# Kernel tuning notes

Measured on AMD Instinct MI355X. Metric: run time of the kernel, lower is better.

## Reference

```python
import jax, jax.numpy as jnp
import numpy as np

NEG_SLOPE = 0.01  # LeakyReLU default


def gcn_conv(x, src, dst, W, b, num_nodes):
    """PyG GCNConv: x' = D^-1/2 (A+I) D^-1/2 (x W) + b, self-loops added."""
    h = x @ W
    loop = jnp.arange(num_nodes)
    s = jnp.concatenate([src, loop])
    d = jnp.concatenate([dst, loop])
    deg = jax.ops.segment_sum(jnp.ones(s.shape[0], dtype=h.dtype), d,
                              num_segments=num_nodes)
    dinv = jnp.where(deg > 0, jax.lax.rsqrt(deg), 0.0)
    norm = dinv[s] * dinv[d]              # (Ep+N,)
    out = jax.ops.segment_sum(h[s] * norm[:, None], d, num_segments=num_nodes)
    return out + b


def leaky_relu(x):
    return jnp.where(x > 0, x, NEG_SLOPE * x)


def setup_inputs() -> dict:
    key = jax.random.key(0)
    ks = jax.random.split(key, 8)
    B, V, E, Fsub, H = 16, 100000, 300000, 800000, 16
    verts = jax.random.normal(ks[0], (B, V, 3), dtype=jnp.float32)
    edges = jax.random.randint(ks[1], (E, 2), 0, V)
    faces_sub = jax.random.randint(ks[2], (Fsub, 3), 0, V + E)
    W1 = jax.random.normal(ks[3], (3, H), dtype=jnp.float32) * 0.01
    W2 = jax.random.normal(ks[4], (H, H), dtype=jnp.float32) * 0.01
    W3 = jax.random.normal(ks[5], (H, 3), dtype=jnp.float32) * 0.01
    return {"verts": verts, "edges": edges, "faces_sub": faces_sub,
            "W1": W1, "b1": jnp.zeros((H,), jnp.float32),
            "W2": W2, "b2": jnp.zeros((H,), jnp.float32),
            "W3": W3, "b3": jnp.zeros((3,), jnp.float32)}


def reference(verts, edges, faces_sub, W1, b1, W2, b2, W3, b3):
    B, V, _ = verts.shape
    E = edges.shape[0]
    N = B * V
    # pack edges across the batch (same topology per mesh, offset per mesh)
    offsets = (jnp.arange(B) * V).astype(edges.dtype)
    pe = (edges[None, :, :] + offsets[:, None, None]).reshape(B * E, 2)
    src, dst = pe[:, 0], pe[:, 1]

    x = verts.reshape(N, 3)
    h = leaky_relu(gcn_conv(x, src, dst, W1, b1, N))
    h = leaky_relu(gcn_conv(h, src, dst, W2, b2, N))
    # Dropout(0.5) is identity at inference
    offs = gcn_conv(h, src, dst, W3, b3, N)

    v = (x + offs).reshape(B, V, 3)          # offset_verts
    mid = v[:, edges].mean(axis=2)           # (B, E, 3) edge midpoints
    new_verts = jnp.concatenate([v, mid], axis=1)   # (B, V+E, 3)
    new_faces = jnp.broadcast_to(faces_sub[None], (B,) + faces_sub.shape)
    return new_verts, new_faces
```

## Files before the change

### kernel.cpp

```cpp
#include <hip/hip_runtime.h>
#include <hip/hip_bf16.h>

#define NEG_SLOPE 0.01f

typedef long long i64;
typedef __hip_bfloat16 bf16;

__device__ __forceinline__ float lrelu(float x) { return x > 0.f ? x : NEG_SLOPE * x; }
__device__ __forceinline__ float b2f(bf16 v) { return __bfloat162float(v); }
__device__ __forceinline__ float lo2f(unsigned u) { return __uint_as_float(u << 16); }
__device__ __forceinline__ float hi2f(unsigned u) { return __uint_as_float(u & 0xffff0000u); }
__device__ __forceinline__ unsigned pk2(float a, float b) {
    unsigned ua = __bfloat16_as_ushort(__float2bfloat16(a));
    unsigned ub = __bfloat16_as_ushort(__float2bfloat16(b));
    return ua | (ub << 16);
}
__device__ __forceinline__ void acc8(float* h, uint4 u) {
    h[0] += lo2f(u.x); h[1] += hi2f(u.x);
    h[2] += lo2f(u.y); h[3] += hi2f(u.y);
    h[4] += lo2f(u.z); h[5] += hi2f(u.z);
    h[6] += lo2f(u.w); h[7] += hi2f(u.w);
}

__device__ __forceinline__ void decode_bxb(int wg, int NB, int CBc, int& b, int& xb) {
    if ((CBc & 7) == 0) {
        int xcd = wg & 7, k = wg >> 3;
        int bl = k / NB;
        xb = k - bl * NB;
        b = xcd + 8 * bl;
    } else {
        b = wg / NB;
        xb = wg - b * NB;
    }
}

__global__ __launch_bounds__(256) void k_deg(const int* __restrict__ edges,
                                             int* __restrict__ indeg, int E) {
    int e = blockIdx.x * 256 + threadIdx.x;
    if (e < E) atomicAdd(&indeg[edges[2 * e + 1]], 1);
}

__global__ __launch_bounds__(256) void k_dinv(const int* __restrict__ indeg,
                                              float* __restrict__ dinv, int V) {
    int v = blockIdx.x * 256 + threadIdx.x;
    if (v < V) dinv[v] = rsqrtf((float)indeg[v] + 1.0f);
}

__global__ __launch_bounds__(256) void k_scan1(const int* __restrict__ indeg,
                                               int* __restrict__ rowptr,
                                               int* __restrict__ bsum, int V) {
    __shared__ int s[256];
    int i = blockIdx.x * 256 + threadIdx.x;
    int x = (i < V) ? indeg[i] : 0;
    s[threadIdx.x] = x;
    __syncthreads();
    for (int off = 1; off < 256; off <<= 1) {
        int t = (threadIdx.x >= (unsigned)off) ? s[threadIdx.x - off] : 0;
        __syncthreads();
        s[threadIdx.x] += t;
        __syncthreads();
    }
    if (i < V) rowptr[i] = s[threadIdx.x] - x;
    if (threadIdx.x == 255) bsum[blockIdx.x] = s[255];
}

__global__ __launch_bounds__(1024) void k_scan2(int* __restrict__ bsum, int NB) {
    __shared__ int s[1024];
    __shared__ int srun;
    if (threadIdx.x == 0) srun = 0;
    __syncthreads();
    for (int base = 0; base < NB; base += 1024) {
        int i = base + threadIdx.x;
        int x = (i < NB) ? bsum[i] : 0;
        s[threadIdx.x] = x;
        __syncthreads();
        for (int off = 1; off < 1024; off <<= 1) {
            int t = (threadIdx.x >= (unsigned)off) ? s[threadIdx.x - off] : 0;
            __syncthreads();
            s[threadIdx.x] += t;
            __syncthreads();
        }
        int run = srun;
        if (i < NB) bsum[i] = run + s[threadIdx.x] - x;
        __syncthreads();
        if (threadIdx.x == 1023) srun = run + s[1023];
        __syncthreads();
    }
}

__global__ __launch_bounds__(256) void k_scan3(int* __restrict__ rowptr,
                                               const int* __restrict__ bsum,
                                               int V, int E) {
    int i = blockIdx.x * 256 + threadIdx.x;
    if (i < V) rowptr[i] += bsum[blockIdx.x];
    if (i == 0) rowptr[V] = E;
}

__global__ __launch_bounds__(256) void k_fill(const int* __restrict__ edges,
                                              const int* __restrict__ rowptr,
                                              int* __restrict__ cur,
                                              int* __restrict__ col, int E) {
    int e = blockIdx.x * 256 + threadIdx.x;
    if (e >= E) return;
    int s = edges[2 * e], d = edges[2 * e + 1];
    int p = atomicAdd(&cur[d], 1);
    col[rowptr[d] + p] = s;
}

__global__ __launch_bounds__(256) void k_gl12(const int* __restrict__ rowptr,
                                              const int* __restrict__ col,
                                              const float* __restrict__ verts,
                                              const float* __restrict__ W1,
                                              const float* __restrict__ b1,
                                              const float* __restrict__ W2,
                                              const float* __restrict__ dinv,
                                              bf16* __restrict__ PB,
                                              float* __restrict__ Q,
                                              int b0, int V, int NB, int CBc) {
    int b, xb;
    decode_bxb(blockIdx.x, NB, CBc, b, xb);
    int v = xb * 256 + threadIdx.x;
    if (v >= V) return;
    i64 vg = (i64)(b0 + b) * V;
    i64 vb = (i64)b * V;
    float di = dinv[v];
    const float* xv = verts + (vg + v) * 3;
    float x0 = xv[0], x1 = xv[1], x2 = xv[2];
    float a0 = di * x0, a1 = di * x1, a2 = di * x2;
    float h[16];
#pragma unroll
    for (int f = 0; f < 16; ++f)
        h[f] = a0 * W1[f] + a1 * W1[16 + f] + a2 * W1[32 + f];
    int r0 = rowptr[v], r1 = rowptr[v + 1];
#pragma unroll 2
    for (int j = r0; j < r1; ++j) {
        int s = col[j];
        float ds = dinv[s];
        const float* xs = verts + (vg + s) * 3;
        float y0 = ds * xs[0], y1 = ds * xs[1], y2 = ds * xs[2];
#pragma unroll
        for (int f = 0; f < 16; ++f)
            h[f] += y0 * W1[f] + y1 * W1[16 + f] + y2 * W1[32 + f];
    }
#pragma unroll
    for (int f = 0; f < 16; ++f) h[f] = lrelu(di * h[f] + b1[f]);
    float g[16];
#pragma unroll
    for (int f = 0; f < 16; ++f) g[f] = 0.f;
#pragma unroll
    for (int k = 0; k < 16; ++k) {
        float hk = h[k];
#pragma unroll
        for (int f = 0; f < 16; ++f) g[f] += hk * W2[k * 16 + f];
    }
#pragma unroll
    for (int f = 0; f < 16; ++f) g[f] *= di;
    i64 m = vb + v;
    uint4* Pp = (uint4*)(PB + m * 16);
    Pp[0] = make_uint4(pk2(g[0], g[1]), pk2(g[2], g[3]), pk2(g[4], g[5]), pk2(g[6], g[7]));
    Pp[1] = make_uint4(pk2(g[8], g[9]), pk2(g[10], g[11]), pk2(g[12], g[13]), pk2(g[14], g[15]));
    float4* Qp = (float4*)(Q + m * 16);
#pragma unroll
    for (int q = 0; q < 4; ++q)
        Qp[q] = make_float4(g[4 * q], g[4 * q + 1], g[4 * q + 2], g[4 * q + 3]);
}

__global__ __launch_bounds__(256) void k_gl3(const int* __restrict__ rowptr,
                                             const int* __restrict__ col,
                                             const float* __restrict__ W3,
                                             const float* __restrict__ b2,
                                             const float* __restrict__ dinv,
                                             const bf16* __restrict__ Pin,
                                             const float* __restrict__ Q,
                                             float* __restrict__ R,
                                             int V, int NB, int CBc) {
    int b, xb;
    decode_bxb(blockIdx.x, NB, CBc, b, xb);
    int v = xb * 256 + threadIdx.x;
    if (v >= V) return;
    i64 vb = (i64)b * V;
    i64 m = vb + v;
    float h[16];
    const float4* Qin = (const float4*)(Q + m * 16);
#pragma unroll
    for (int q = 0; q < 4; ++q) {
        float4 t = Qin[q];
        h[4 * q] = t.x; h[4 * q + 1] = t.y; h[4 * q + 2] = t.z; h[4 * q + 3] = t.w;
    }
    const uint4* Pb = (const uint4*)(Pin + vb * 16);
    int r0 = rowptr[v], r1 = rowptr[v + 1];
    int j = r0;
    for (; j + 1 < r1; j += 2) {
        size_t u0 = (size_t)col[j] * 2, u1 = (size_t)col[j + 1] * 2;
        uint4 q0 = Pb[u0], q1 = Pb[u0 + 1];
        uint4 c0 = Pb[u1], c1 = Pb[u1 + 1];
        acc8(h, q0); acc8(h + 8, q1);
        acc8(h, c0); acc8(h + 8, c1);
    }
    if (j < r1) {
        size_t u0 = (size_t)col[j] * 2;
        uint4 q0 = Pb[u0], q1 = Pb[u0 + 1];
        acc8(h, q0); acc8(h + 8, q1);
    }
    float di = dinv[v];
    float g0 = 0.f, g1 = 0.f, g2 = 0.f;
#pragma unroll
    for (int k = 0; k < 16; ++k) {
        float hk = lrelu(di * h[k] + b2[k]);
        g0 += hk * W3[k * 3 + 0];
        g1 += hk * W3[k * 3 + 1];
        g2 += hk * W3[k * 3 + 2];
    }
    ((float4*)R)[m] = make_float4(di * g0, di * g1, di * g2, 0.f);
}

__global__ __launch_bounds__(256) void k_gvert(const int* __restrict__ rowptr,
                                               const int* __restrict__ col,
                                               const float* __restrict__ x,
                                               const float* __restrict__ b3,
                                               const float* __restrict__ dinv,
                                               const float* __restrict__ R,
                                               float* __restrict__ Vpos,
                                               float* __restrict__ out0,
                                               int b0, int V, int E, int NB, int CBc) {
    int b, xb;
    decode_bxb(blockIdx.x, NB, CBc, b, xb);
    int v = xb * 256 + threadIdx.x;
    if (v >= V) return;
    i64 vb = (i64)b * V;
    i64 m = vb + v;
    const float4* Rb = (const float4*)R + vb;
    float4 s = Rb[v];
    int r0 = rowptr[v], r1 = rowptr[v + 1];
    int j = r0;
    for (; j + 1 < r1; j += 2) {
        float4 t0 = Rb[col[j]];
        float4 t1 = Rb[col[j + 1]];
        s.x += t0.x + t1.x; s.y += t0.y + t1.y; s.z += t0.z + t1.z;
    }
    if (j < r1) {
        float4 t0 = Rb[col[j]];
        s.x += t0.x; s.y += t0.y; s.z += t0.z;
    }
    float di = dinv[v];
    int bg = b0 + b;
    i64 n = (i64)bg * V + v;
    float p0 = x[n * 3]     + di * s.x + b3[0];
    float p1 = x[n * 3 + 1] + di * s.y + b3[1];
    float p2 = x[n * 3 + 2] + di * s.z + b3[2];
    ((float4*)Vpos)[m] = make_float4(p0, p1, p2, 0.f);
    i64 o = ((i64)bg * (V + E) + v) * 3;
    __builtin_nontemporal_store(p0, out0 + o);
    __builtin_nontemporal_store(p1, out0 + o + 1);
    __builtin_nontemporal_store(p2, out0 + o + 2);
}

__global__ __launch_bounds__(256) void k_mid(const int* __restrict__ edges,
                                             const float* __restrict__ Vpos,
                                             float* __restrict__ out0,
                                             int b0, int V, int E, int NB, int CBc) {
    int b, xe;
    decode_bxb(blockIdx.x, NB, CBc, b, xe);
    int e = xe * 256 + threadIdx.x;
    if (e >= E) return;
    int s = edges[2 * e], d = edges[2 * e + 1];
    float4 ps = ((const float4*)Vpos)[(i64)b * V + s];
    float4 pd = ((const float4*)Vpos)[(i64)b * V + d];
    i64 o = ((i64)(b0 + b) * (V + E) + V + e) * 3;
    __builtin_nontemporal_store(0.5f * (ps.x + pd.x), out0 + o);
    __builtin_nontemporal_store(0.5f * (ps.y + pd.y), out0 + o + 1);
    __builtin_nontemporal_store(0.5f * (ps.z + pd.z), out0 + o + 2);
}

__global__ __launch_bounds__(256) void k_faces(const int* __restrict__ faces,
                                               float* __restrict__ out1,
                                               i64 F3, i64 faceElems) {
    i64 i = (i64)blockIdx.x * 256 + threadIdx.x;
    if (i >= F3) return;
    i64 o = (i64)blockIdx.y * F3 + i;
    if (o < faceElems) __builtin_nontemporal_store((float)faces[i], out1 + o);
}

__global__ __launch_bounds__(256) void k_l1_g(const float* __restrict__ x,
                                              const float* __restrict__ W1,
                                              const float* __restrict__ dinv,
                                              bf16* __restrict__ P, float* __restrict__ Q,
                                              int b0, int V, int H) {
    extern __shared__ float sW[];
    for (int i = threadIdx.x; i < 3 * H; i += 256) sW[i] = W1[i];
    __syncthreads();
    int v = blockIdx.x * 256 + threadIdx.x;
    if (v >= V) return;
    i64 n = (i64)(b0 + blockIdx.y) * V + v;
    i64 m = (i64)blockIdx.y * V + v;
    float di = dinv[v];
    float x0 = x[n * 3], x1 = x[n * 3 + 1], x2 = x[n * 3 + 2];
    for (int f = 0; f < H; ++f) {
        float g = di * (x0 * sW[f] + x1 * sW[H + f] + x2 * sW[2 * H + f]);
        P[m * H + f] = __float2bfloat16(g);
        Q[m * H + f] = g;
    }
}

__global__ __launch_bounds__(256) void k_scatter_g(const int* __restrict__ edges,
                                                   const bf16* __restrict__ P,
                                                   float* __restrict__ Q,
                                                   int E, int V, int H) {
    int e = blockIdx.x * 256 + threadIdx.x;
    if (e >= E) return;
    int b = blockIdx.y;
    int s = edges[2 * e], d = edges[2 * e + 1];
    for (int f = 0; f < H; ++f)
        unsafeAtomicAdd(&Q[((i64)b * V + d) * H + f], b2f(P[((i64)b * V + s) * H + f]));
}

__global__ __launch_bounds__(256) void k_l2_g(const float* __restrict__ W2,
                                              const float* __restrict__ b1,
                                              const float* __restrict__ dinv,
                                              bf16* __restrict__ P, float* __restrict__ Q,
                                              int V, int H) {
    extern __shared__ float sW[];
    float* sb = sW + H * H;
    for (int i = threadIdx.x; i < H * H; i += 256) sW[i] = W2[i];
    for (int i = threadIdx.x; i < H; i += 256) sb[i] = b1[i];
    __syncthreads();
    int v = blockIdx.x * 256 + threadIdx.x;
    if (v >= V) return;
    i64 m = (i64)blockIdx.y * V + v;
    float di = dinv[v];
    float h[64];
    for (int k = 0; k < H; ++k) h[k] = lrelu(di * Q[m * H + k] + sb[k]);
    for (int f = 0; f < H; ++f) {
        float a = 0.f;
        for (int k = 0; k < H; ++k) a += h[k] * sW[k * H + f];
        float g = di * a;
        P[m * H + f] = __float2bfloat16(g);
        Q[m * H + f] = g;
    }
}

__global__ __launch_bounds__(256) void k_l3_g(const float* __restrict__ W3,
                                              const float* __restrict__ b2,
                                              const float* __restrict__ dinv,
                                              float* __restrict__ R,
                                              const float* __restrict__ Q, int V, int H) {
    extern __shared__ float sW[];
    float* sb = sW + H * 3;
    for (int i = threadIdx.x; i < H * 3; i += 256) sW[i] = W3[i];
    for (int i = threadIdx.x; i < H; i += 256) sb[i] = b2[i];
    __syncthreads();
    int v = blockIdx.x * 256 + threadIdx.x;
    if (v >= V) return;
    i64 m = (i64)blockIdx.y * V + v;
    float di = dinv[v];
    float g0 = 0.f, g1 = 0.f, g2 = 0.f;
    for (int k = 0; k < H; ++k) {
        float h = lrelu(di * Q[m * H + k] + sb[k]);
        g0 += h * sW[k * 3]; g1 += h * sW[k * 3 + 1]; g2 += h * sW[k * 3 + 2];
    }
    ((float4*)R)[m] = make_float4(di * g0, di * g1, di * g2, 0.f);
}

extern "C" void kernel_launch(void* const* d_in, const int* in_sizes, int n_in,
                              void* d_out, int out_size, void* d_ws, size_t ws_size,
                              hipStream_t stream) {
    const float* verts = (const float*)d_in[0];
    const int*   edges = (const int*)d_in[1];
    const int*   faces = (const int*)d_in[2];
    const float* W1 = (const float*)d_in[3];
    const float* b1 = (const float*)d_in[4];
    const float* W2 = (const float*)d_in[5];
    const float* b2 = (const float*)d_in[6];
    const float* W3 = (const float*)d_in[7];
    const float* b3 = (const float*)d_in[8];

    const i64 s0 = in_sizes[0];
    const i64 E  = in_sizes[1] / 2;
    const i64 F  = in_sizes[2] / 3;
    const int H  = in_sizes[4];
    i64 B = 0;
    const i64 denomB = 3 * (E + F);
    if ((i64)out_size > s0 && denomB > 0) {
        i64 Bc = ((i64)out_size - s0) / denomB;
        if (Bc >= 1 && s0 + Bc * denomB == (i64)out_size && s0 % (3 * Bc) == 0) B = Bc;
    }
    if (B == 0) {
        i64 num = (i64)out_size - s0 - 3 * F;
        if (num > 0 && E > 0 && num % (3 * E) == 0) {
            i64 Bc = num / (3 * E);
            if (Bc >= 1 && s0 % (3 * Bc) == 0) B = Bc;
        }
    }
    if (B == 0) B = 16;
    const i64 V = s0 / (3 * B);

    const i64 Vp  = (V + 255) & ~255LL;
    const i64 NB1 = Vp >> 8;
    const size_t AUX = (size_t)Vp * 4  + (size_t)Vp * 4
                     + (size_t)(Vp + 256) * 4
                     + (size_t)(NB1 + 256) * 4
                     + (size_t)E * 4  + 1024;
    const size_t rowB = (size_t)(6 * H) + 96 + 64;
    i64 CB = B;
    while (CB > 1 && AUX + (size_t)CB * V * rowB + 8192 > ws_size) CB = (CB + 1) / 2;

    float* ws     = (float*)d_ws;
    float* dinv   = ws;
    int*   indeg  = (int*)(ws + Vp);
    int*   rowptr = indeg + Vp;
    int*   bsum   = rowptr + Vp + 256;
    int*   col    = bsum + NB1 + 256;
    char*  base   = (char*)(((size_t)(col + E) + 255) & ~(size_t)255);
    auto pad = [](size_t x) { return (x + 255) & ~(size_t)255; };

    bf16 *PB = nullptr, *Pg = nullptr;
    float *Q, *R, *Vb;
    {
        char* p = base;
        if (H == 16) {
            PB = (bf16*)p;  p += pad((size_t)CB * V * 32);
            Q  = (float*)p; p += pad((size_t)CB * V * 64);
        } else {
            Pg = (bf16*)p;  p += pad((size_t)CB * V * 2 * H);
            Q  = (float*)p; p += pad((size_t)CB * V * 4 * H);
        }
        R  = (float*)p; p += pad((size_t)CB * V * 16);
        Vb = (float*)p;
    }

    const unsigned NBv = (unsigned)((V + 255) / 256);
    const unsigned NBe = (unsigned)((E + 255) / 256);

    hipMemsetAsync(indeg, 0, V * sizeof(int), stream);
    if (NBe) k_deg<<<dim3(NBe), 256, 0, stream>>>(edges, indeg, (int)E);
    k_dinv<<<dim3(NBv), 256, 0, stream>>>(indeg, dinv, (int)V);
    k_scan1<<<dim3(NBv), 256, 0, stream>>>(indeg, rowptr, bsum, (int)V);
    k_scan2<<<dim3(1), 1024, 0, stream>>>(bsum, (int)NBv);
    k_scan3<<<dim3(NBv), 256, 0, stream>>>(rowptr, bsum, (int)V, (int)E);
    hipMemsetAsync(indeg, 0, V * sizeof(int), stream);
    if (NBe) k_fill<<<dim3(NBe), 256, 0, stream>>>(edges, rowptr, indeg, col, (int)E);

    float* out0 = (float*)d_out;
    const i64 vertElems = B * (V + E) * 3;
    float* out1 = out0 + vertElems;
    const i64 faceElems = (i64)out_size - vertElems;

    for (i64 b0 = 0; b0 < B; b0 += CB) {
        const i64 CBc = (B - b0 < CB) ? (B - b0) : CB;
        dim3 g1((unsigned)(NBv * CBc));
        dim3 g1e((unsigned)(NBe * CBc));
        if (H == 16) {
            k_gl12<<<g1, 256, 0, stream>>>(rowptr, col, verts, W1, b1, W2, dinv,
                                           PB, Q, (int)b0, (int)V, (int)NBv, (int)CBc);
            k_gl3<<<g1, 256, 0, stream>>>(rowptr, col, W3, b2, dinv, PB, Q, R,
                                          (int)V, (int)NBv, (int)CBc);
        } else {
            dim3 gn(NBv, (unsigned)CBc);
            dim3 ge(NBe, (unsigned)CBc);
            size_t sh1 = (size_t)3 * H * 4;
            size_t sh2 = ((size_t)H * H + H) * 4;
            size_t sh3 = ((size_t)H * 3 + H) * 4;
            k_l1_g<<<gn, 256, sh1, stream>>>(verts, W1, dinv, Pg, Q, (int)b0, (int)V, H);
            if (NBe) k_scatter_g<<<ge, 256, 0, stream>>>(edges, Pg, Q, (int)E, (int)V, H);
            k_l2_g<<<gn, 256, sh2, stream>>>(W2, b1, dinv, Pg, Q, (int)V, H);
            if (NBe) k_scatter_g<<<ge, 256, 0, stream>>>(edges, Pg, Q, (int)E, (int)V, H);
            k_l3_g<<<gn, 256, sh3, stream>>>(W3, b2, dinv, R, Q, (int)V, H);
        }
        k_gvert<<<g1, 256, 0, stream>>>(rowptr, col, verts, b3, dinv, R, Vb, out0,
                                        (int)b0, (int)V, (int)E, (int)NBv, (int)CBc);
        if (NBe) k_mid<<<g1e, 256, 0, stream>>>(edges, Vb, out0, (int)b0, (int)V, (int)E,
                                                (int)NBe, (int)CBc);
    }
    const i64 F3 = 3 * F;
    if (faceElems > 0 && F3 > 0)
        k_faces<<<dim3((unsigned)((F3 + 255) / 256), (unsigned)B), 256, 0, stream>>>(
            faces, out1, F3, faceElems);
}
```

Measured before the change: 534.2 us.

## Process four batch meshes per thread to reuse CSR neighbor indices

Each thread in the fused layer kernels, the vertex-update kernel and the midpoint kernel now handles up to four batch meshes for the same vertex or edge. The shared rowptr/col/dinv loads are read once and reused across those meshes. Layer 1 now aggregates the raw 3-dim coordinates before multiplying by W1, which cuts per-neighbor FLOPs from 48 to 3 per mesh. The XCD-aware block remapping is dropped in favour of a 2D grid, and registers per thread rise with four sets of accumulators.

```diff
diff --git a/kernel.cpp b/kernel.cpp
--- a/kernel.cpp
+++ b/kernel.cpp
@@ -20,18 +20,6 @@
     h[2] += lo2f(u.y); h[3] += hi2f(u.y);
     h[4] += lo2f(u.z); h[5] += hi2f(u.z);
     h[6] += lo2f(u.w); h[7] += hi2f(u.w);
-}
-
-__device__ __forceinline__ void decode_bxb(int wg, int NB, int CBc, int& b, int& xb) {
-    if ((CBc & 7) == 0) {
-        int xcd = wg & 7, k = wg >> 3;
-        int bl = k / NB;
-        xb = k - bl * NB;
-        b = xcd + 8 * bl;
-    } else {
-        b = wg / NB;
-        xb = wg - b * NB;
-    }
 }
 
 __global__ __launch_bounds__(256) void k_deg(const int* __restrict__ edges,
@@ -116,53 +104,62 @@
                                               const float* __restrict__ dinv,
                                               bf16* __restrict__ PB,
                                               float* __restrict__ Q,
-                                              int b0, int V, int NB, int CBc) {
-    int b, xb;
-    decode_bxb(blockIdx.x, NB, CBc, b, xb);
-    int v = xb * 256 + threadIdx.x;
-    if (v >= V) return;
-    i64 vg = (i64)(b0 + b) * V;
-    i64 vb = (i64)b * V;
-    float di = dinv[v];
-    const float* xv = verts + (vg + v) * 3;
-    float x0 = xv[0], x1 = xv[1], x2 = xv[2];
-    float a0 = di * x0, a1 = di * x1, a2 = di * x2;
-    float h[16];
-#pragma unroll
-    for (int f = 0; f < 16; ++f)
-        h[f] = a0 * W1[f] + a1 * W1[16 + f] + a2 * W1[32 + f];
+                                              int b0, int V, int CBc) {
+    int v = blockIdx.x * 256 + threadIdx.x;
+    if (v >= V) return;
+    int bg0 = blockIdx.y * 4;
+    int nb = CBc - bg0; if (nb > 4) nb = 4;
+    float di = dinv[v];
+    i64 gvb[4];
+#pragma unroll
+    for (int mb = 0; mb < 4; ++mb) {
+        int mbc = mb < nb ? mb : nb - 1;
+        gvb[mb] = (i64)(b0 + bg0 + mbc) * V;
+    }
+    float c[4][3];
+#pragma unroll
+    for (int mb = 0; mb < 4; ++mb) {
+        const float* xv = verts + (gvb[mb] + v) * 3;
+        c[mb][0] = di * xv[0]; c[mb][1] = di * xv[1]; c[mb][2] = di * xv[2];
+    }
     int r0 = rowptr[v], r1 = rowptr[v + 1];
-#pragma unroll 2
     for (int j = r0; j < r1; ++j) {
         int s = col[j];
         float ds = dinv[s];
-        const float* xs = verts + (vg + s) * 3;
-        float y0 = ds * xs[0], y1 = ds * xs[1], y2 = ds * xs[2];
+#pragma unroll
+        for (int mb = 0; mb < 4; ++mb) {
+            const float* xs = verts + (gvb[mb] + s) * 3;
+            c[mb][0] += ds * xs[0]; c[mb][1] += ds * xs[1]; c[mb][2] += ds * xs[2];
+        }
+    }
+#pragma unroll
+    for (int mb = 0; mb < 4; ++mb) {
+        if (mb >= nb) break;
+        float h[16];
 #pragma unroll
         for (int f = 0; f < 16; ++f)
-            h[f] += y0 * W1[f] + y1 * W1[16 + f] + y2 * W1[32 + f];
-    }
-#pragma unroll
-    for (int f = 0; f < 16; ++f) h[f] = lrelu(di * h[f] + b1[f]);
-    float g[16];
-#pragma unroll
-    for (int f = 0; f < 16; ++f) g[f] = 0.f;
-#pragma unroll
-    for (int k = 0; k < 16; ++k) {
-        float hk = h[k];
-#pragma unroll
-        for (int f = 0; f < 16; ++f) g[f] += hk * W2[k * 16 + f];
-    }
-#pragma unroll
-    for (int f = 0; f < 16; ++f) g[f] *= di;
-    i64 m = vb + v;
-    uint4* Pp = (uint4*)(PB + m * 16);
-    Pp[0] = make_uint4(pk2(g[0], g[1]), pk2(g[2], g[3]), pk2(g[4], g[5]), pk2(g[6], g[7]));
-    Pp[1] = make_uint4(pk2(g[8], g[9]), pk2(g[10], g[11]), pk2(g[12], g[13]), pk2(g[14], g[15]));
-    float4* Qp = (float4*)(Q + m * 16);
-#pragma unroll
-    for (int q = 0; q < 4; ++q)
-        Qp[q] = make_float4(g[4 * q], g[4 * q + 1], g[4 * q + 2], g[4 * q + 3]);
+            h[f] = lrelu(di * (c[mb][0] * W1[f] + c[mb][1] * W1[16 + f] +
+                               c[mb][2] * W1[32 + f]) + b1[f]);
+        float g[16];
+#pragma unroll
+        for (int f = 0; f < 16; ++f) g[f] = 0.f;
+#pragma unroll
+        for (int k = 0; k < 16; ++k) {
+            float hk = h[k];
+#pragma unroll
+            for (int f = 0; f < 16; ++f) g[f] += hk * W2[k * 16 + f];
+        }
+#pragma unroll
+        for (int f = 0; f < 16; ++f) g[f] *= di;
+        i64 m = (i64)(bg0 + mb) * V + v;
+        uint4* Pp = (uint4*)(PB + m * 16);
+        Pp[0] = make_uint4(pk2(g[0], g[1]), pk2(g[2], g[3]), pk2(g[4], g[5]), pk2(g[6], g[7]));
+        Pp[1] = make_uint4(pk2(g[8], g[9]), pk2(g[10], g[11]), pk2(g[12], g[13]), pk2(g[14], g[15]));
+        float4* Qp = (float4*)(Q + m * 16);
+#pragma unroll
+        for (int q = 0; q < 4; ++q)
+            Qp[q] = make_float4(g[4 * q], g[4 * q + 1], g[4 * q + 2], g[4 * q + 3]);
+    }
 }
 
 __global__ __launch_bounds__(256) void k_gl3(const int* __restrict__ rowptr,
@@ -173,45 +170,52 @@
                                              const bf16* __restrict__ Pin,
                                              const float* __restrict__ Q,
                                              float* __restrict__ R,
-                                             int V, int NB, int CBc) {
-    int b, xb;
-    decode_bxb(blockIdx.x, NB, CBc, b, xb);
-    int v = xb * 256 + threadIdx.x;
-    if (v >= V) return;
-    i64 vb = (i64)b * V;
-    i64 m = vb + v;
-    float h[16];
-    const float4* Qin = (const float4*)(Q + m * 16);
-#pragma unroll
-    for (int q = 0; q < 4; ++q) {
-        float4 t = Qin[q];
-        h[4 * q] = t.x; h[4 * q + 1] = t.y; h[4 * q + 2] = t.z; h[4 * q + 3] = t.w;
-    }
-    const uint4* Pb = (const uint4*)(Pin + vb * 16);
+                                             int V, int CBc) {
+    int v = blockIdx.x * 256 + threadIdx.x;
+    if (v >= V) return;
+    int bg0 = blockIdx.y * 4;
+    int nb = CBc - bg0; if (nb > 4) nb = 4;
+    i64 vb[4];
+#pragma unroll
+    for (int mb = 0; mb < 4; ++mb) {
+        int mbc = mb < nb ? mb : nb - 1;
+        vb[mb] = (i64)(bg0 + mbc) * V;
+    }
+    float h[4][16];
+#pragma unroll
+    for (int mb = 0; mb < 4; ++mb) {
+        const float4* Qin = (const float4*)(Q + (vb[mb] + v) * 16);
+#pragma unroll
+        for (int q = 0; q < 4; ++q) {
+            float4 t = Qin[q];
+            h[mb][4 * q] = t.x; h[mb][4 * q + 1] = t.y;
+            h[mb][4 * q + 2] = t.z; h[mb][4 * q + 3] = t.w;
+        }
+    }
     int r0 = rowptr[v], r1 = rowptr[v + 1];
-    int j = r0;
-    for (; j + 1 < r1; j += 2) {
-        size_t u0 = (size_t)col[j] * 2, u1 = (size_t)col[j + 1] * 2;
-        uint4 q0 = Pb[u0], q1 = Pb[u0 + 1];
-        uint4 c0 = Pb[u1], c1 = Pb[u1 + 1];
-        acc8(h, q0); acc8(h + 8, q1);
-        acc8(h, c0); acc8(h + 8, c1);
-    }
-    if (j < r1) {
-        size_t u0 = (size_t)col[j] * 2;
-        uint4 q0 = Pb[u0], q1 = Pb[u0 + 1];
-        acc8(h, q0); acc8(h + 8, q1);
-    }
-    float di = dinv[v];
-    float g0 = 0.f, g1 = 0.f, g2 = 0.f;
-#pragma unroll
-    for (int k = 0; k < 16; ++k) {
-        float hk = lrelu(di * h[k] + b2[k]);
-        g0 += hk * W3[k * 3 + 0];
-        g1 += hk * W3[k * 3 + 1];
-        g2 += hk * W3[k * 3 + 2];
-    }
-    ((float4*)R)[m] = make_float4(di * g0, di * g1, di * g2, 0.f);
+    for (int j = r0; j < r1; ++j) {
+        size_t u = (size_t)col[j] * 2;
+#pragma unroll
+        for (int mb = 0; mb < 4; ++mb) {
+            const uint4* Pb = (const uint4*)(Pin + vb[mb] * 16);
+            uint4 q0 = Pb[u], q1 = Pb[u + 1];
+            acc8(h[mb], q0); acc8(h[mb] + 8, q1);
+        }
+    }
+    float di = dinv[v];
+#pragma unroll
+    for (int mb = 0; mb < 4; ++mb) {
+        if (mb >= nb) break;
+        float g0 = 0.f, g1 = 0.f, g2 = 0.f;
+#pragma unroll
+        for (int k = 0; k < 16; ++k) {
+            float hk = lrelu(di * h[mb][k] + b2[k]);
+            g0 += hk * W3[k * 3 + 0];
+            g1 += hk * W3[k * 3 + 1];
+            g2 += hk * W3[k * 3 + 2];
+        }
+        ((float4*)R)[vb[mb] + v] = make_float4(di * g0, di * g1, di * g2, 0.f);
+    }
 }
 
 __global__ __launch_bounds__(256) void k_gvert(const int* __restrict__ rowptr,
@@ -222,54 +226,66 @@
                                                const float* __restrict__ R,
                                                float* __restrict__ Vpos,
                                                float* __restrict__ out0,
-                                               int b0, int V, int E, int NB, int CBc) {
-    int b, xb;
-    decode_bxb(blockIdx.x, NB, CBc, b, xb);
-    int v = xb * 256 + threadIdx.x;
-    if (v >= V) return;
-    i64 vb = (i64)b * V;
-    i64 m = vb + v;
-    const float4* Rb = (const float4*)R + vb;
-    float4 s = Rb[v];
+                                               int b0, int V, int E, int CBc) {
+    int v = blockIdx.x * 256 + threadIdx.x;
+    if (v >= V) return;
+    int bg0 = blockIdx.y * 4;
+    int nb = CBc - bg0; if (nb > 4) nb = 4;
+    i64 vb[4];
+#pragma unroll
+    for (int mb = 0; mb < 4; ++mb) {
+        int mbc = mb < nb ? mb : nb - 1;
+        vb[mb] = (i64)(bg0 + mbc) * V;
+    }
+    float4 s[4];
+#pragma unroll
+    for (int mb = 0; mb < 4; ++mb) s[mb] = ((const float4*)R)[vb[mb] + v];
     int r0 = rowptr[v], r1 = rowptr[v + 1];
-    int j = r0;
-    for (; j + 1 < r1; j += 2) {
-        float4 t0 = Rb[col[j]];
-        float4 t1 = Rb[col[j + 1]];
-        s.x += t0.x + t1.x; s.y += t0.y + t1.y; s.z += t0.z + t1.z;
-    }
-    if (j < r1) {
-        float4 t0 = Rb[col[j]];
-        s.x += t0.x; s.y += t0.y; s.z += t0.z;
-    }
-    float di = dinv[v];
-    int bg = b0 + b;
-    i64 n = (i64)bg * V + v;
-    float p0 = x[n * 3]     + di * s.x + b3[0];
-    float p1 = x[n * 3 + 1] + di * s.y + b3[1];
-    float p2 = x[n * 3 + 2] + di * s.z + b3[2];
-    ((float4*)Vpos)[m] = make_float4(p0, p1, p2, 0.f);
-    i64 o = ((i64)bg * (V + E) + v) * 3;
-    __builtin_nontemporal_store(p0, out0 + o);
-    __builtin_nontemporal_store(p1, out0 + o + 1);
-    __builtin_nontemporal_store(p2, out0 + o + 2);
+    for (int j = r0; j < r1; ++j) {
+        int cs = col[j];
+#pragma unroll
+        for (int mb = 0; mb < 4; ++mb) {
+            float4 t = ((const float4*)R)[vb[mb] + cs];
+            s[mb].x += t.x; s[mb].y += t.y; s[mb].z += t.z;
+        }
+    }
+    float di = dinv[v];
+#pragma unroll
+    for (int mb = 0; mb < 4; ++mb) {
+        if (mb >= nb) break;
+        int bg = b0 + bg0 + mb;
+        i64 n = (i64)bg * V + v;
+        float p0 = x[n * 3]     + di * s[mb].x + b3[0];
+        float p1 = x[n * 3 + 1] + di * s[mb].y + b3[1];
+        float p2 = x[n * 3 + 2] + di * s[mb].z + b3[2];
+        ((float4*)Vpos)[vb[mb] + v] = make_float4(p0, p1, p2, 0.f);
+        i64 o = ((i64)bg * (V + E) + v) * 3;
+        __builtin_nontemporal_store(p0, out0 + o);
+        __builtin_nontemporal_store(p1, out0 + o + 1);
+        __builtin_nontemporal_store(p2, out0 + o + 2);
+    }
 }
 
 __global__ __launch_bounds__(256) void k_mid(const int* __restrict__ edges,
                                              const float* __restrict__ Vpos,
                                              float* __restrict__ out0,
-                                             int b0, int V, int E, int NB, int CBc) {
-    int b, xe;
-    decode_bxb(blockIdx.x, NB, CBc, b, xe);
-    int e = xe * 256 + threadIdx.x;
+                                             int b0, int V, int E, int CBc) {
+    int e = blockIdx.x * 256 + threadIdx.x;
     if (e >= E) return;
+    int bg0 = blockIdx.y * 4;
+    int nb = CBc - bg0; if (nb > 4) nb = 4;
     int s = edges[2 * e], d = edges[2 * e + 1];
-    float4 ps = ((const float4*)Vpos)[(i64)b * V + s];
-    float4 pd = ((const float4*)Vpos)[(i64)b * V + d];
-    i64 o = ((i64)(b0 + b) * (V + E) + V + e) * 3;
-    __builtin_nontemporal_store(0.5f * (ps.x + pd.x), out0 + o);
-    __builtin_nontemporal_store(0.5f * (ps.y + pd.y), out0 + o + 1);
-    __builtin_nontemporal_store(0.5f * (ps.z + pd.z), out0 + o + 2);
+#pragma unroll
+    for (int mb = 0; mb < 4; ++mb) {
+        if (mb >= nb) break;
+        i64 vb = (i64)(bg0 + mb) * V;
+        float4 ps = ((const float4*)Vpos)[vb + s];
+        float4 pd = ((const float4*)Vpos)[vb + d];
+        i64 o = ((i64)(b0 + bg0 + mb) * (V + E) + V + e) * 3;
+        __builtin_nontemporal_store(0.5f * (ps.x + pd.x), out0 + o);
+        __builtin_nontemporal_store(0.5f * (ps.y + pd.y), out0 + o + 1);
+        __builtin_nontemporal_store(0.5f * (ps.z + pd.z), out0 + o + 2);
+    }
 }
 
 __global__ __launch_bounds__(256) void k_faces(const int* __restrict__ faces,
@@ -359,6 +375,52 @@
         g0 += h * sW[k * 3]; g1 += h * sW[k * 3 + 1]; g2 += h * sW[k * 3 + 2];
     }
     ((float4*)R)[m] = make_float4(di * g0, di * g1, di * g2, 0.f);
+}
+
+__global__ __launch_bounds__(256) void k_gvert_g(const int* __restrict__ rowptr,
+                                                 const int* __restrict__ col,
+                                                 const float* __restrict__ x,
+                                                 const float* __restrict__ b3,
+                                                 const float* __restrict__ dinv,
+                                                 const float* __restrict__ R,
+                                                 float* __restrict__ Vpos,
+                                                 float* __restrict__ out0,
+                                                 int b0, int V, int E) {
+    int v = blockIdx.x * 256 + threadIdx.x;
+    if (v >= V) return;
+    int b = blockIdx.y;
+    i64 vb = (i64)b * V;
+    const float4* Rb = (const float4*)R + vb;
+    float4 s = Rb[v];
+    int r0 = rowptr[v], r1 = rowptr[v + 1];
+    for (int j = r0; j < r1; ++j) {
+        float4 t = Rb[col[j]];
+        s.x += t.x; s.y += t.y; s.z += t.z;
+    }
+    float di = dinv[v];
+    int bg = b0 + b;
+    i64 n = (i64)bg * V + v;
+    float p0 = x[n * 3]     + di * s.x + b3[0];
+    float p1 = x[n * 3 + 1] + di * s.y + b3[1];
+    float p2 = x[n * 3 + 2] + di * s.z + b3[2];
+    ((float4*)Vpos)[vb + v] = make_float4(p0, p1, p2, 0.f);
+    i64 o = ((i64)bg * (V + E) + v) * 3;
+    out0[o] = p0; out0[o + 1] = p1; out0[o + 2] = p2;
+}
+
+__global__ __launch_bounds__(256) void k_mid_g(const int* __restrict__ edges,
+                                               const float* __restrict__ Vpos,
+                                               float* __restrict__ out0,
+                                               int b0, int V, int E) {
+    int e = blockIdx.x * 256 + threadIdx.x;
+    if (e >= E) return;
+    int s = edges[2 * e], d = edges[2 * e + 1];
+    float4 ps = ((const float4*)Vpos)[(i64)blockIdx.y * V + s];
+    float4 pd = ((const float4*)Vpos)[(i64)blockIdx.y * V + d];
+    i64 o = ((i64)(b0 + blockIdx.y) * (V + E) + V + e) * 3;
+    out0[o]     = 0.5f * (ps.x + pd.x);
+    out0[o + 1] = 0.5f * (ps.y + pd.y);
+    out0[o + 2] = 0.5f * (ps.z + pd.z);
 }
 
 extern "C" void kernel_launch(void* const* d_in, const int* in_sizes, int n_in,
@@ -447,13 +509,18 @@
 
     for (i64 b0 = 0; b0 < B; b0 += CB) {
         const i64 CBc = (B - b0 < CB) ? (B - b0) : CB;
-        dim3 g1((unsigned)(NBv * CBc));
-        dim3 g1e((unsigned)(NBe * CBc));
         if (H == 16) {
-            k_gl12<<<g1, 256, 0, stream>>>(rowptr, col, verts, W1, b1, W2, dinv,
-                                           PB, Q, (int)b0, (int)V, (int)NBv, (int)CBc);
-            k_gl3<<<g1, 256, 0, stream>>>(rowptr, col, W3, b2, dinv, PB, Q, R,
-                                          (int)V, (int)NBv, (int)CBc);
+            const unsigned NG = (unsigned)((CBc + 3) / 4);
+            dim3 gn(NBv, NG);
+            dim3 ge(NBe, NG);
+            k_gl12<<<gn, 256, 0, stream>>>(rowptr, col, verts, W1, b1, W2, dinv,
+                                           PB, Q, (int)b0, (int)V, (int)CBc);
+            k_gl3<<<gn, 256, 0, stream>>>(rowptr, col, W3, b2, dinv, PB, Q, R,
+                                          (int)V, (int)CBc);
+            k_gvert<<<gn, 256, 0, stream>>>(rowptr, col, verts, b3, dinv, R, Vb, out0,
+                                            (int)b0, (int)V, (int)E, (int)CBc);
+            if (NBe) k_mid<<<ge, 256, 0, stream>>>(edges, Vb, out0, (int)b0, (int)V,
+                                                   (int)E, (int)CBc);
         } else {
             dim3 gn(NBv, (unsigned)CBc);
             dim3 ge(NBe, (unsigned)CBc);
@@ -465,11 +532,11 @@
             k_l2_g<<<gn, 256, sh2, stream>>>(W2, b1, dinv, Pg, Q, (int)V, H);
             if (NBe) k_scatter_g<<<ge, 256, 0, stream>>>(edges, Pg, Q, (int)E, (int)V, H);
             k_l3_g<<<gn, 256, sh3, stream>>>(W3, b2, dinv, R, Q, (int)V, H);
-        }
-        k_gvert<<<g1, 256, 0, stream>>>(rowptr, col, verts, b3, dinv, R, Vb, out0,
-                                        (int)b0, (int)V, (int)E, (int)NBv, (int)CBc);
-        if (NBe) k_mid<<<g1e, 256, 0, stream>>>(edges, Vb, out0, (int)b0, (int)V, (int)E,
-                                                (int)NBe, (int)CBc);
+            k_gvert_g<<<gn, 256, 0, stream>>>(rowptr, col, verts, b3, dinv, R, Vb, out0,
+                                              (int)b0, (int)V, (int)E);
+            if (NBe) k_mid_g<<<ge, 256, 0, stream>>>(edges, Vb, out0, (int)b0, (int)V,
+                                                     (int)E);
+        }
     }
     const i64 F3 = 3 * F;
     if (faceElems > 0 && F3 > 0)
```

New measurement: 686.1 us. 28.4% more time.
